# Kernel tuning notes

Hardware: AMD Instinct MI355X
Metric: run time of the kernel (lower is better)

## Reference

```python
import jax, jax.numpy as jnp
import numpy as np

EPS = 1e-5


def setup_inputs() -> dict:
    key = jax.random.key(0)
    ks = jax.random.split(key, 10)
    B, C, H, W = 4, 256, 64, 64
    x = jax.random.normal(ks[0], (B, C, H, W), dtype=jnp.float32)
    s = 1.0 / np.sqrt(C)
    inp = {
        "x": x,
        "gn_w": jnp.ones((C,), jnp.float32),
        "gn_b": jnp.zeros((C,), jnp.float32),
        "wq": jax.random.normal(ks[1], (C, C), jnp.float32) * s,
        "bq": jnp.zeros((C,), jnp.float32),
        "wk": jax.random.normal(ks[2], (C, C), jnp.float32) * s,
        "bk": jnp.zeros((C,), jnp.float32),
        "wv": jax.random.normal(ks[3], (C, C), jnp.float32) * s,
        "bv": jnp.zeros((C,), jnp.float32),
        "wo": jax.random.normal(ks[4], (C, C), jnp.float32) * s,
        "bo": jnp.zeros((C,), jnp.float32),
    }
    return inp


def _forward(x, gn_w, gn_b, wq, bq, wk, bk, wv, bv, wo, bo):
    B, C, H, W = x.shape
    G = C // 2  # num_groups = channels // 2 -> 2 channels per group
    # GroupNorm
    xg = x.reshape(B, G, C // G, H, W)
    mu = jnp.mean(xg, axis=(2, 3, 4), keepdims=True)
    var = jnp.var(xg, axis=(2, 3, 4), keepdims=True)
    hn = ((xg - mu) * jax.lax.rsqrt(var + EPS)).reshape(B, C, H, W)
    hn = hn * gn_w[None, :, None, None] + gn_b[None, :, None, None]
    # tokens: (B, N, C), N = H*W
    h = hn.transpose(0, 2, 3, 1).reshape(B, H * W, C)
    q = h @ wq.T + bq
    k = h @ wk.T + bk
    v = h @ wv.T + bv
    # full NxN attention, scaled by C^-0.5 (as in original)
    scores = jnp.einsum("bnc,bmc->bnm", q, k) * (C ** -0.5)
    attn = jax.nn.softmax(scores, axis=-1)
    h2 = jnp.einsum("bnm,bmc->bnc", attn, v)  # (B, N, C)
    # faithful replication of the original's layout-scrambling reshape:
    # (B,N,C) -> (B,H,W,C) -> permute (B,C,H,W) -> reshape (B,HW,C)
    h2 = h2.reshape(B, H, W, C).transpose(0, 3, 1, 2).reshape(B, H * W, C)
    out = (h2 @ wo.T + bo).reshape(B, C, H, W)
    return x + out


def reference(x, gn_w, gn_b, wq, bq, wk, bk, wv, bv, wo, bo):
    return _forward(x, gn_w, gn_b, wq, bq, wk, bk, wv, bv, wo, bo)
```

## Files before the change

### kernel.cpp

```cpp
#include <hip/hip_runtime.h>

typedef unsigned short u16;
typedef unsigned int   u32;
typedef __attribute__((ext_vector_type(8)))  short short8;
typedef __attribute__((ext_vector_type(4)))  float f32x4;
typedef __attribute__((ext_vector_type(16))) float f32x16;

#define DI __device__ __forceinline__

DI u16 f2bf(float f){
  u32 u = __builtin_bit_cast(u32, f);
  u += 0x7fffu + ((u >> 16) & 1u);
  return (u16)(u >> 16);
}

DI void gl_lds16(const void* g, void* l){
  __builtin_amdgcn_global_load_lds((const __attribute__((address_space(1))) void*)g,
                                   (__attribute__((address_space(3))) void*)l, 16, 0, 0);
}

DI f32x4 mfma16(short8 a, short8 b, f32x4 c){
  return __builtin_amdgcn_mfma_f32_16x16x32_bf16(a, b, c, 0, 0, 0);
}
DI f32x16 mfma32(short8 a, short8 b, f32x16 c){
  return __builtin_amdgcn_mfma_f32_32x32x16_bf16(a, b, c, 0, 0, 0);
}
DI f32x16 z16(){
  f32x16 v;
  #pragma unroll
  for (int i=0;i<16;i++) v[i]=0.f;
  return v;
}

union U8 { u32 u[4]; short8 s; };

#define OFF_WBF   0u
#define OFF_STATS (512u<<10)
#define OFF_HTOK  (1u<<20)
#define OFF_Q     ((1u<<20) + (8u<<20))
#define OFF_K     ((1u<<20) + (16u<<20))
#define OFF_VT    ((1u<<20) + (24u<<20))
#define OFF_H2T   OFF_Q
#define OFF_PART  ((1u<<20) + (32u<<20))
#define OFF_ML    ((1u<<20) + (96u<<20))

__global__ void k_prep(const float* w0, const float* w1, const float* w2, const float* w3, u16* wbf){
  const float* src = (blockIdx.y==0)?w0:(blockIdx.y==1)?w1:(blockIdx.y==2)?w2:w3;
  u16* d = wbf + blockIdx.y*65536;
  int i = (blockIdx.x*256 + threadIdx.x)*4;
  float4 v = *(const float4*)(src + i);
  u32 lo = (u32)f2bf(v.x) | ((u32)f2bf(v.y)<<16);
  u32 hi = (u32)f2bf(v.z) | ((u32)f2bf(v.w)<<16);
  *(uint2*)(d + i) = make_uint2(lo, hi);
}

__global__ void k_gnstats(const float* x, float2* stats){
  int bg = blockIdx.x;
  const float* p = x + (size_t)bg*8192;
  float s = 0.f, ss = 0.f;
  #pragma unroll
  for (int i=0;i<8;i++){
    float4 v = *(const float4*)(p + threadIdx.x*4 + i*1024);
    s  += v.x+v.y+v.z+v.w;
    ss += v.x*v.x + v.y*v.y + v.z*v.z + v.w*v.w;
  }
  #pragma unroll
  for (int off=1; off<64; off<<=1){ s += __shfl_xor(s, off, 64); ss += __shfl_xor(ss, off, 64); }
  __shared__ float as[4], aq[4];
  int w = threadIdx.x>>6;
  if ((threadIdx.x&63)==0){ as[w]=s; aq[w]=ss; }
  __syncthreads();
  if (threadIdx.x==0){
    s = as[0]+as[1]+as[2]+as[3]; ss = aq[0]+aq[1]+aq[2]+aq[3];
    float mu = s * (1.f/8192.f);
    float var = ss * (1.f/8192.f) - mu*mu;
    stats[bg] = make_float2(mu, rsqrtf(var + 1e-5f));
  }
}

__global__ void k_gnapply(const float* x, const float* gw, const float* gb,
                          const float2* stats, u16* htok){
  __shared__ u16 tile[64*256];
  int b = blockIdx.y, n0 = blockIdx.x*64, t = threadIdx.x;
  const float* xb = x + (size_t)b*1048576;
  #pragma unroll
  for (int p=0;p<4;p++){
    int c = p*64 + (t>>2);
    float2 st = stats[b*128 + (c>>1)];
    float scl = st.y * gw[c];
    float off = gb[c] - st.x*scl;
    const float* src = xb + (size_t)c*4096 + n0 + (t&3)*16;
    #pragma unroll
    for (int u2=0;u2<4;u2++){
      float4 v = *(const float4*)(src + u2*4);
      float vv[4] = {v.x,v.y,v.z,v.w};
      #pragma unroll
      for (int j=0;j<4;j++){
        int n = (t&3)*16 + u2*4 + j;
        int addr = n*512 + ((c*2) ^ ((n&7)<<4));
        *(u16*)((char*)tile + addr) = f2bf(vv[j]*scl + off);
      }
    }
  }
  __syncthreads();
  int n = t>>2, seg = t&3;
  char* dst = (char*)(htok + ((size_t)(b*4096 + n0 + n)*256 + seg*64));
  #pragma unroll
  for (int i=0;i<8;i++){
    int boff = n*512 + (((seg*128) + i*16) ^ ((n&7)<<4));
    *(uint4*)(dst + i*16) = *(const uint4*)((const char*)tile + boff);
  }
}

__global__ __launch_bounds__(256,2) void k_qkv(const u16* htok, const u16* wbf,
    const float* bq, const float* bk, const float* bv,
    u16* qo, u16* ko, u16* vt){
  __shared__ u16 lds_a[64*256];
  const int t = threadIdx.x, row0 = blockIdx.x*64;
  const int w = t>>6, l = t&63, lo = l&15, hi = l>>4;
  {
    const char* Ab = (const char*)htok + (size_t)row0*512;
    #pragma unroll
    for (int i=0;i<8;i++){
      int row = w*16 + i*2 + (l>>5);
      gl_lds16(Ab + row*512 + (((l&31)*16) ^ ((row&7)<<4)), lds_a + w*4096 + i*512);
    }
    __syncthreads();
  }
  auto compute = [&](const u16* W, f32x4 acc[4][4]){
    #pragma unroll
    for (int i=0;i<4;i++)
      #pragma unroll
      for (int j=0;j<4;j++) acc[i][j] = (f32x4){0.f,0.f,0.f,0.f};
    const char* Wb = (const char*)W;
    #pragma unroll
    for (int dk=0; dk<4; dk++){
      #pragma unroll
      for (int s=0;s<2;s++){
        short8 af[4], bf[4];
        #pragma unroll
        for (int cf=0;cf<4;cf++){
          int col = w*64 + cf*16 + lo;
          bf[cf] = *(const short8*)(Wb + (size_t)col*512 + dk*128 + s*64 + hi*16);
        }
        #pragma unroll
        for (int rg=0;rg<4;rg++){
          int row = rg*16 + lo;
          af[rg] = *(const short8*)((const char*)lds_a + row*512 + ((dk*128 + s*64 + hi*16) ^ ((row&7)<<4)));
        }
        #pragma unroll
        for (int rg=0;rg<4;rg++)
          #pragma unroll
          for (int cf=0;cf<4;cf++)
            acc[rg][cf] = mfma16(af[rg], bf[cf], acc[rg][cf]);
      }
    }
  };
  f32x4 acc[4][4];
  compute(wbf, acc);
  #pragma unroll
  for (int rg=0;rg<4;rg++)
    #pragma unroll
    for (int cf=0;cf<4;cf++){
      int col = w*64 + cf*16 + lo;
      float bs = bq[col];
      #pragma unroll
      for (int r=0;r<4;r++){
        int grow = row0 + rg*16 + hi*4 + r;
        qo[(size_t)grow*256 + col] = f2bf((acc[rg][cf][r] + bs)*0.09016844f);
      }
    }
  compute(wbf + 65536, acc);
  #pragma unroll
  for (int rg=0;rg<4;rg++)
    #pragma unroll
    for (int cf=0;cf<4;cf++){
      int col = w*64 + cf*16 + lo;
      float bs = bk[col];
      #pragma unroll
      for (int r=0;r<4;r++){
        int grow = row0 + rg*16 + hi*4 + r;
        ko[(size_t)grow*256 + col] = f2bf(acc[rg][cf][r] + bs);
      }
    }
  compute(wbf + 2*65536, acc);
  __syncthreads();
  #pragma unroll
  for (int rg=0;rg<4;rg++)
    #pragma unroll
    for (int cf=0;cf<4;cf++){
      int col = w*64 + cf*16 + lo;
      float bs = bv[col];
      ushort4 pk;
      pk.x = f2bf(acc[rg][cf][0]+bs); pk.y = f2bf(acc[rg][cf][1]+bs);
      pk.z = f2bf(acc[rg][cf][2]+bs); pk.w = f2bf(acc[rg][cf][3]+bs);
      int rl = rg*16 + hi*4;
      int addr = col*128 + ((rl*2) ^ ((col&7)<<4));
      *(ushort4*)((char*)lds_a + addr) = pk;
    }
  __syncthreads();
  {
    int b = row0 >> 12, nb = row0 & 4095;
    #pragma unroll
    for (int p=0;p<8;p++){
      int c = p*32 + (t>>3), i = t&7;
      uint4 vd = *(const uint4*)((const char*)lds_a + c*128 + ((i*16) ^ ((c&7)<<4)));
      *(uint4*)((char*)vt + ((size_t)(b*256 + c)*4096 + nb)*2 + i*16) = vd;
    }
  }
}

__global__ __launch_bounds__(256,2) void k_out(const u16* h2t, const u16* wo,
    const float* bo, const float* x, float* out){
  __shared__ u16 lds_a[64*256];
  const int t = threadIdx.x, row0 = blockIdx.x*64;
  const int w = t>>6, l = t&63, lo = l&15, hi = l>>4;
  {
    const char* Ab = (const char*)h2t + (size_t)row0*512;
    #pragma unroll
    for (int i=0;i<8;i++){
      int row = w*16 + i*2 + (l>>5);
      gl_lds16(Ab + row*512 + (((l&31)*16) ^ ((row&7)<<4)), lds_a + w*4096 + i*512);
    }
    __syncthreads();
  }
  f32x4 acc[4][4];
  #pragma unroll
  for (int i=0;i<4;i++)
    #pragma unroll
    for (int j=0;j<4;j++) acc[i][j] = (f32x4){0.f,0.f,0.f,0.f};
  const char* Wb = (const char*)wo;
  #pragma unroll
  for (int dk=0; dk<4; dk++){
    #pragma unroll
    for (int s=0;s<2;s++){
      short8 af[4], bf[4];
      #pragma unroll
      for (int cf=0;cf<4;cf++){
        int col = w*64 + cf*16 + lo;
        bf[cf] = *(const short8*)(Wb + (size_t)col*512 + dk*128 + s*64 + hi*16);
      }
      #pragma unroll
      for (int rg=0;rg<4;rg++){
        int row = rg*16 + lo;
        af[rg] = *(const short8*)((const char*)lds_a + row*512 + ((dk*128 + s*64 + hi*16) ^ ((row&7)<<4)));
      }
      #pragma unroll
      for (int rg=0;rg<4;rg++)
        #pragma unroll
        for (int cf=0;cf<4;cf++)
          acc[rg][cf] = mfma16(af[rg], bf[cf], acc[rg][cf]);
    }
  }
  #pragma unroll
  for (int rg=0;rg<4;rg++)
    #pragma unroll
    for (int cf=0;cf<4;cf++){
      int col = w*64 + cf*16 + lo;
      float bs = bo[col];
      #pragma unroll
      for (int r=0;r<4;r++){
        size_t flat = (size_t)(row0 + rg*16 + hi*4 + r)*256 + col;
        out[flat] = x[flat] + acc[rg][cf][r] + bs;
      }
    }
}

__global__ __launch_bounds__(512,2) void k_attn(const u16* q, const u16* k,
                                                const u16* vt, u16* part, float2* ml){
  __shared__ char smem[131072];
  const int t = threadIdx.x, w = t>>6, l = t&63;
  const int lq = l&31, h = l>>5;
  const int bid = blockIdx.x;
  const int x = bid&7, idx = bid>>3;
  const int combo = x*2 + (idx&1);
  const int b = combo>>2, ks = combo&3, qt = idx>>1;

  const char* kg = (const char*)k  + ((size_t)b*4096 + (size_t)ks*1024)*512;
  const char* vg = (const char*)vt + (size_t)b*2097152 + (size_t)ks*2048;

  short8 qf[16];
  {
    const char* qrow = (const char*)q + ((size_t)b*4096 + qt*256 + w*32 + lq)*512;
    #pragma unroll
    for (int dk=0;dk<16;dk++) qf[dk] = *(const short8*)(qrow + dk*32 + h*16);
  }

  f32x16 O[8];
  #pragma unroll
  for (int ct=0;ct<8;ct++) O[ct] = z16();
  float m_run = -1e30f, l_run = 0.f;

  auto stage = [&](int ti, int buf){
    #pragma unroll
    for (int sub=0; sub<2; ++sub){
      char* kd = smem + buf*32768 + sub*16384;
      char* vd = smem + 65536 + buf*32768 + sub*16384;
      #pragma unroll
      for (int j=0;j<2;j++){
        int key = w*4 + j*2 + h;
        gl_lds16(kg + (size_t)(ti*64 + sub*32 + key)*512 + (((l&31)*16) ^ ((key&7)<<4)),
                 kd + (w*2+j)*1024);
      }
      #pragma unroll
      for (int j=0;j<2;j++){
        int c = w*32 + j*16 + (l>>2);
        gl_lds16(vg + (size_t)c*8192 + ti*128 + sub*64 + (((l&3)*16) ^ (((l>>3)&3)<<4)),
                 vd + (w*2+j)*1024);
      }
    }
  };

  stage(0, 0);
  __syncthreads();

  for (int tile=0; tile<16; ++tile){
    const int cur = tile&1;
    if (tile < 15) stage(tile+1, cur^1);
    const char* kbuf0 = smem + cur*32768;
    const char* kbuf1 = kbuf0 + 16384;
    const char* vbuf0 = smem + 65536 + cur*32768;
    const char* vbuf1 = vbuf0 + 16384;

    f32x16 S0 = z16(), S1 = z16();
    __builtin_amdgcn_s_setprio(1);
    #pragma unroll
    for (int dk=0;dk<16;dk++){
      int dby = (dk*32 + h*16) ^ ((lq&7)<<4);
      short8 k0 = *(const short8*)(kbuf0 + (size_t)lq*512 + dby);
      short8 k1 = *(const short8*)(kbuf1 + (size_t)lq*512 + dby);
      S0 = mfma32(k0, qf[dk], S0);
      S1 = mfma32(k1, qf[dk], S1);
    }
    __builtin_amdgcn_s_setprio(0);

    float pmax = fmaxf(S0[0], S1[0]);
    #pragma unroll
    for (int r=1;r<16;r++) pmax = fmaxf(pmax, fmaxf(S0[r], S1[r]));
    pmax = fmaxf(pmax, __shfl_xor(pmax, 32, 64));
    if (__any(pmax > m_run + 8.f)){
      float mn = fmaxf(m_run, pmax);
      float sclq = exp2f(m_run - mn);
      m_run = mn;
      l_run *= sclq;
      #pragma unroll
      for (int r=0;r<16;r++){
        float sr = __shfl(sclq, (r&3)+8*(r>>2)+4*h, 64);
        #pragma unroll
        for (int ct=0;ct<8;ct++) O[ct][r] *= sr;
      }
    }
    float ps = 0.f;
    u32 pk0[8], pk1[8];
    #pragma unroll
    for (int j=0;j<8;j++){
      float p0 = exp2f(S0[2*j]   - m_run);
      float p1 = exp2f(S0[2*j+1] - m_run);
      ps += p0 + p1;
      pk0[j] = (__builtin_bit_cast(u32, p1) & 0xffff0000u) | (__builtin_bit_cast(u32, p0) >> 16);
    }
    #pragma unroll
    for (int j=0;j<8;j++){
      float p0 = exp2f(S1[2*j]   - m_run);
      float p1 = exp2f(S1[2*j+1] - m_run);
      ps += p0 + p1;
      pk1[j] = (__builtin_bit_cast(u32, p1) & 0xffff0000u) | (__builtin_bit_cast(u32, p0) >> 16);
    }
    l_run += ps + __shfl_xor(ps, 32, 64);

    U8 pa00, pa01, pa10, pa11;
    #pragma unroll
    for (int kc=0;kc<2;kc++){
      {
        u32 sA = h ? pk0[4*kc]   : pk0[4*kc+2];
        u32 sB = h ? pk0[4*kc+1] : pk0[4*kc+3];
        u32 xA = __shfl_xor(sA, 32, 64);
        u32 xB = __shfl_xor(sB, 32, 64);
        U8& pa = kc ? pa01 : pa00;
        pa.u[0] = h ? xA : pk0[4*kc];
        pa.u[1] = h ? xB : pk0[4*kc+1];
        pa.u[2] = h ? pk0[4*kc+2] : xA;
        pa.u[3] = h ? pk0[4*kc+3] : xB;
      }
      {
        u32 sA = h ? pk1[4*kc]   : pk1[4*kc+2];
        u32 sB = h ? pk1[4*kc+1] : pk1[4*kc+3];
        u32 xA = __shfl_xor(sA, 32, 64);
        u32 xB = __shfl_xor(sB, 32, 64);
        U8& pa = kc ? pa11 : pa10;
        pa.u[0] = h ? xA : pk1[4*kc];
        pa.u[1] = h ? xB : pk1[4*kc+1];
        pa.u[2] = h ? pk1[4*kc+2] : xA;
        pa.u[3] = h ? pk1[4*kc+3] : xB;
      }
    }
    __builtin_amdgcn_s_setprio(1);
    #pragma unroll
    for (int kc=0;kc<2;kc++){
      #pragma unroll
      for (int ct=0;ct<8;ct++){
        short8 vb = *(const short8*)(vbuf0 + (size_t)(ct*32+lq)*64 + ((kc*32 + h*16) ^ (((lq>>1)&3)<<4)));
        O[ct] = mfma32(kc ? pa01.s : pa00.s, vb, O[ct]);
      }
    }
    #pragma unroll
    for (int kc=0;kc<2;kc++){
      #pragma unroll
      for (int ct=0;ct<8;ct++){
        short8 vb = *(const short8*)(vbuf1 + (size_t)(ct*32+lq)*64 + ((kc*32 + h*16) ^ (((lq>>1)&3)<<4)));
        O[ct] = mfma32(kc ? pa11.s : pa10.s, vb, O[ct]);
      }
    }
    __builtin_amdgcn_s_setprio(0);
    __syncthreads();
  }

  if (h == 0)
    ml[(size_t)combo*4096 + qt*256 + w*32 + lq] = make_float2(m_run, l_run);
  u16* otile = (u16*)smem;
  char* pbase = (char*)part + ((size_t)combo*4096 + (size_t)qt*256)*512;
  #pragma unroll
  for (int rd=0; rd<2; ++rd){
    __syncthreads();
    if ((w>>2) == rd){
      int wl = w&3;
      #pragma unroll
      for (int ct=0;ct<8;ct++)
        #pragma unroll
        for (int r=0;r<16;r++){
          int row = wl*32 + (r&3) + 8*(r>>2) + 4*h;
          otile[row*256 + ct*32 + lq] = f2bf(O[ct][r]);
        }
    }
    __syncthreads();
    const char* sb2 = (const char*)smem;
    char* gb2 = pbase + (size_t)rd*65536;
    #pragma unroll
    for (int j=0;j<8;j++)
      *(uint4*)(gb2 + t*16 + (size_t)j*8192) = *(const uint4*)(sb2 + t*16 + (size_t)j*8192);
  }
}

__global__ __launch_bounds__(256,2) void k_combine(const u16* part, const float2* ml, u16* h2t){
  __shared__ u16 tile[64*256];
  const int t = threadIdx.x, b = blockIdx.y, n0 = blockIdx.x*64;
  const int n = t>>2, cc = (t&3)*64;
  const int gn = n0 + n;
  float2 st[4]; float ms = -1e30f;
  #pragma unroll
  for (int ksi=0;ksi<4;ksi++){ st[ksi] = ml[(size_t)(b*4+ksi)*4096 + gn]; ms = fmaxf(ms, st[ksi].x); }
  float wn[4]; float denom = 0.f;
  #pragma unroll
  for (int ksi=0;ksi<4;ksi++){ wn[ksi] = exp2f(st[ksi].x - ms); denom += wn[ksi]*st[ksi].y; }
  float inv = 1.f/denom;
  #pragma unroll
  for (int ksi=0;ksi<4;ksi++) wn[ksi] *= inv;
  float acc[64];
  #pragma unroll
  for (int j=0;j<64;j++) acc[j] = 0.f;
  #pragma unroll
  for (int ksi=0;ksi<4;ksi++){
    const u16* src = part + ((size_t)(b*4+ksi)*4096 + gn)*256 + cc;
    float wv = wn[ksi];
    #pragma unroll
    for (int j8=0;j8<8;j8++){
      short8 v = *(const short8*)(src + j8*8);
      #pragma unroll
      for (int e=0;e<8;e++){
        u32 uu = ((u32)(u16)v[e])<<16;
        acc[j8*8+e] += wv * __builtin_bit_cast(float, uu);
      }
    }
  }
  char* tb = (char*)tile;
  #pragma unroll
  for (int j=0;j<32;j++){
    u32 pkv = ((u32)f2bf(acc[2*j+1])<<16) | f2bf(acc[2*j]);
    *(u32*)(tb + n*512 + ((cc*2 + j*4) ^ ((n&7)<<4))) = pkv;
  }
  __syncthreads();
  {
    const char* tbc = (const char*)tile;
    u32 outw[32];
    #pragma unroll
    for (int j=0;j<32;j++){
      u16 v0 = *(const u16*)(tbc + (2*j  )*512 + ((t*2) ^ (((2*j  )&7)<<4)));
      u16 v1 = *(const u16*)(tbc + (2*j+1)*512 + ((t*2) ^ (((2*j+1)&7)<<4)));
      outw[j] = ((u32)v1<<16) | v0;
    }
    char* dst = (char*)h2t + ((size_t)(b*256 + t)*4096 + n0)*2;
    #pragma unroll
    for (int j=0;j<8;j++){
      uint4 vv; vv.x = outw[4*j]; vv.y = outw[4*j+1]; vv.z = outw[4*j+2]; vv.w = outw[4*j+3];
      *(uint4*)(dst + j*16) = vv;
    }
  }
}

extern "C" void kernel_launch(void* const* d_in, const int* in_sizes, int n_in,
                              void* d_out, int out_size, void* d_ws, size_t ws_size,
                              hipStream_t stream) {
  const float* x    = (const float*)d_in[0];
  const float* gn_w = (const float*)d_in[1];
  const float* gn_b = (const float*)d_in[2];
  const float* wq   = (const float*)d_in[3];
  const float* bq   = (const float*)d_in[4];
  const float* wk   = (const float*)d_in[5];
  const float* bk   = (const float*)d_in[6];
  const float* wv   = (const float*)d_in[7];
  const float* bv   = (const float*)d_in[8];
  const float* wo   = (const float*)d_in[9];
  const float* bo   = (const float*)d_in[10];
  float* out = (float*)d_out;
  char* ws = (char*)d_ws;

  u16*    wbf   = (u16*)(ws + OFF_WBF);
  float2* stats = (float2*)(ws + OFF_STATS);
  u16*    htok  = (u16*)(ws + OFF_HTOK);
  u16*    qb    = (u16*)(ws + OFF_Q);
  u16*    kb    = (u16*)(ws + OFF_K);
  u16*    vt    = (u16*)(ws + OFF_VT);
  u16*    h2t   = (u16*)(ws + OFF_H2T);
  u16*    part  = (u16*)(ws + OFF_PART);
  float2* ml    = (float2*)(ws + OFF_ML);

  k_prep   <<<dim3(64,4), 256, 0, stream>>>(wq, wk, wv, wo, wbf);
  k_gnstats<<<512,        256, 0, stream>>>(x, stats);
  k_gnapply<<<dim3(64,4), 256, 0, stream>>>(x, gn_w, gn_b, stats, htok);
  k_qkv    <<<256,        256, 0, stream>>>(htok, wbf, bq, bk, bv, qb, kb, vt);
  k_attn   <<<256,        512, 0, stream>>>(qb, kb, vt, part, ml);
  k_combine<<<dim3(64,4), 256, 0, stream>>>(part, ml, h2t);
  k_out    <<<256,        256, 0, stream>>>(h2t, wbf + 3*65536, bo, x, out);
}
```

Measured before the change: 184.6 us.

## Software-pipeline QK^T of next key subtile with softmax/PV of current

The attention main loop switches from 16 double-buffered 64-key tiles to 32 key subtiles of 32 keys held in a 4-slot LDS ring buffer. Staging runs up to three subtiles ahead. The QK^T MFMAs for subtile i+1 are issued alongside the softmax and PV work for subtile i, so matrix and vector/exp work can interleave. The aim is to hide the softmax latency between the two MFMA phases. In exchange, the online max and rescale check runs twice as often, and the s_setprio hints are dropped.

```diff
diff --git a/kernel.cpp b/kernel.cpp
--- a/kernel.cpp
+++ b/kernel.cpp
@@ -291,52 +291,38 @@
   for (int ct=0;ct<8;ct++) O[ct] = z16();
   float m_run = -1e30f, l_run = 0.f;
 
-  auto stage = [&](int ti, int buf){
-    #pragma unroll
-    for (int sub=0; sub<2; ++sub){
-      char* kd = smem + buf*32768 + sub*16384;
-      char* vd = smem + 65536 + buf*32768 + sub*16384;
-      #pragma unroll
-      for (int j=0;j<2;j++){
-        int key = w*4 + j*2 + h;
-        gl_lds16(kg + (size_t)(ti*64 + sub*32 + key)*512 + (((l&31)*16) ^ ((key&7)<<4)),
-                 kd + (w*2+j)*1024);
-      }
-      #pragma unroll
-      for (int j=0;j<2;j++){
-        int c = w*32 + j*16 + (l>>2);
-        gl_lds16(vg + (size_t)c*8192 + ti*128 + sub*64 + (((l&3)*16) ^ (((l>>3)&3)<<4)),
-                 vd + (w*2+j)*1024);
-      }
+  auto stage = [&](int sub){
+    char* kd = smem + (sub&3)*16384;
+    char* vd = smem + 65536 + (sub&3)*16384;
+    #pragma unroll
+    for (int j=0;j<2;j++){
+      int key = w*4 + j*2 + h;
+      gl_lds16(kg + (size_t)(sub*32 + key)*512 + (((l&31)*16) ^ ((key&7)<<4)),
+               kd + (w*2+j)*1024);
+    }
+    #pragma unroll
+    for (int j=0;j<2;j++){
+      int c = w*32 + j*16 + (l>>2);
+      gl_lds16(vg + (size_t)c*8192 + sub*64 + (((l&3)*16) ^ (((l>>3)&3)<<4)),
+               vd + (w*2+j)*1024);
     }
   };
 
-  stage(0, 0);
-  __syncthreads();
-
-  for (int tile=0; tile<16; ++tile){
-    const int cur = tile&1;
-    if (tile < 15) stage(tile+1, cur^1);
-    const char* kbuf0 = smem + cur*32768;
-    const char* kbuf1 = kbuf0 + 16384;
-    const char* vbuf0 = smem + 65536 + cur*32768;
-    const char* vbuf1 = vbuf0 + 16384;
-
-    f32x16 S0 = z16(), S1 = z16();
-    __builtin_amdgcn_s_setprio(1);
+  auto qkt = [&](int sub, f32x16& S){
+    const char* kbuf = smem + (sub&3)*16384;
+    S = z16();
     #pragma unroll
     for (int dk=0;dk<16;dk++){
-      int dby = (dk*32 + h*16) ^ ((lq&7)<<4);
-      short8 k0 = *(const short8*)(kbuf0 + (size_t)lq*512 + dby);
-      short8 k1 = *(const short8*)(kbuf1 + (size_t)lq*512 + dby);
-      S0 = mfma32(k0, qf[dk], S0);
-      S1 = mfma32(k1, qf[dk], S1);
-    }
-    __builtin_amdgcn_s_setprio(0);
-
-    float pmax = fmaxf(S0[0], S1[0]);
-    #pragma unroll
-    for (int r=1;r<16;r++) pmax = fmaxf(pmax, fmaxf(S0[r], S1[r]));
+      short8 kf = *(const short8*)(kbuf + (size_t)lq*512 + ((dk*32 + h*16) ^ ((lq&7)<<4)));
+      S = mfma32(kf, qf[dk], S);
+    }
+  };
+
+  auto smpv = [&](int sub, const f32x16& S){
+    const char* vbuf = smem + 65536 + (sub&3)*16384;
+    float pmax = S[0];
+    #pragma unroll
+    for (int r=1;r<16;r++) pmax = fmaxf(pmax, S[r]);
     pmax = fmaxf(pmax, __shfl_xor(pmax, 32, 64));
     if (__any(pmax > m_run + 8.f)){
       float mn = fmaxf(m_run, pmax);
@@ -350,70 +336,53 @@
         for (int ct=0;ct<8;ct++) O[ct][r] *= sr;
       }
     }
-    float ps = 0.f;
-    u32 pk0[8], pk1[8];
+    float p[16]; float ps = 0.f;
+    #pragma unroll
+    for (int r=0;r<16;r++){ p[r] = exp2f(S[r] - m_run); ps += p[r]; }
+    l_run += ps + __shfl_xor(ps, 32, 64);
+    u32 pk[8];
     #pragma unroll
     for (int j=0;j<8;j++){
-      float p0 = exp2f(S0[2*j]   - m_run);
-      float p1 = exp2f(S0[2*j+1] - m_run);
-      ps += p0 + p1;
-      pk0[j] = (__builtin_bit_cast(u32, p1) & 0xffff0000u) | (__builtin_bit_cast(u32, p0) >> 16);
-    }
-    #pragma unroll
-    for (int j=0;j<8;j++){
-      float p0 = exp2f(S1[2*j]   - m_run);
-      float p1 = exp2f(S1[2*j+1] - m_run);
-      ps += p0 + p1;
-      pk1[j] = (__builtin_bit_cast(u32, p1) & 0xffff0000u) | (__builtin_bit_cast(u32, p0) >> 16);
-    }
-    l_run += ps + __shfl_xor(ps, 32, 64);
-
-    U8 pa00, pa01, pa10, pa11;
+      u32 u0 = __builtin_bit_cast(u32, p[2*j]);
+      u32 u1 = __builtin_bit_cast(u32, p[2*j+1]);
+      pk[j] = (u1 & 0xffff0000u) | (u0 >> 16);
+    }
     #pragma unroll
     for (int kc=0;kc<2;kc++){
-      {
-        u32 sA = h ? pk0[4*kc]   : pk0[4*kc+2];
-        u32 sB = h ? pk0[4*kc+1] : pk0[4*kc+3];
-        u32 xA = __shfl_xor(sA, 32, 64);
-        u32 xB = __shfl_xor(sB, 32, 64);
-        U8& pa = kc ? pa01 : pa00;
-        pa.u[0] = h ? xA : pk0[4*kc];
-        pa.u[1] = h ? xB : pk0[4*kc+1];
-        pa.u[2] = h ? pk0[4*kc+2] : xA;
-        pa.u[3] = h ? pk0[4*kc+3] : xB;
-      }
-      {
-        u32 sA = h ? pk1[4*kc]   : pk1[4*kc+2];
-        u32 sB = h ? pk1[4*kc+1] : pk1[4*kc+3];
-        u32 xA = __shfl_xor(sA, 32, 64);
-        u32 xB = __shfl_xor(sB, 32, 64);
-        U8& pa = kc ? pa11 : pa10;
-        pa.u[0] = h ? xA : pk1[4*kc];
-        pa.u[1] = h ? xB : pk1[4*kc+1];
-        pa.u[2] = h ? pk1[4*kc+2] : xA;
-        pa.u[3] = h ? pk1[4*kc+3] : xB;
-      }
-    }
-    __builtin_amdgcn_s_setprio(1);
-    #pragma unroll
-    for (int kc=0;kc<2;kc++){
+      u32 sA = h ? pk[4*kc]   : pk[4*kc+2];
+      u32 sB = h ? pk[4*kc+1] : pk[4*kc+3];
+      u32 xA = __shfl_xor(sA, 32, 64);
+      u32 xB = __shfl_xor(sB, 32, 64);
+      U8 pa;
+      pa.u[0] = h ? xA : pk[4*kc];
+      pa.u[1] = h ? xB : pk[4*kc+1];
+      pa.u[2] = h ? pk[4*kc+2] : xA;
+      pa.u[3] = h ? pk[4*kc+3] : xB;
       #pragma unroll
       for (int ct=0;ct<8;ct++){
-        short8 vb = *(const short8*)(vbuf0 + (size_t)(ct*32+lq)*64 + ((kc*32 + h*16) ^ (((lq>>1)&3)<<4)));
-        O[ct] = mfma32(kc ? pa01.s : pa00.s, vb, O[ct]);
-      }
-    }
-    #pragma unroll
-    for (int kc=0;kc<2;kc++){
-      #pragma unroll
-      for (int ct=0;ct<8;ct++){
-        short8 vb = *(const short8*)(vbuf1 + (size_t)(ct*32+lq)*64 + ((kc*32 + h*16) ^ (((lq>>1)&3)<<4)));
-        O[ct] = mfma32(kc ? pa11.s : pa10.s, vb, O[ct]);
-      }
-    }
-    __builtin_amdgcn_s_setprio(0);
+        short8 vb = *(const short8*)(vbuf + (size_t)(ct*32+lq)*64 + ((kc*32 + h*16) ^ (((lq>>1)&3)<<4)));
+        O[ct] = mfma32(pa.s, vb, O[ct]);
+      }
+    }
+  };
+
+  f32x16 SA, SB;
+  stage(0); stage(1); stage(2);
+  __syncthreads();
+  qkt(0, SA);
+  for (int it=0; it<30; it+=2){
+    stage(it+3);
+    qkt(it+1, SB);
+    smpv(it, SA);
     __syncthreads();
-  }
+    if (it+4 < 32) stage(it+4);
+    qkt(it+2, SA);
+    smpv(it+1, SB);
+    __syncthreads();
+  }
+  qkt(31, SB);
+  smpv(30, SA);
+  smpv(31, SB);
 
   if (h == 0)
     ml[(size_t)combo*4096 + qt*256 + w*32 + lq] = make_float2(m_run, l_run);
```

Result: no change. 185.6 us (+0.5%).
